# Optimization experiments

Measured on AMD Instinct MI355X. Metric: run time of the kernel, lower is better.

## Reference

```python
import jax, jax.numpy as jnp
import numpy as np

EPS = 1e-12  # matches torch F.normalize default eps

def setup_inputs() -> dict:
    key = jax.random.key(0)
    x = jax.random.normal(key, (8192, 512), dtype=jnp.float32)
    return {"x": x}

def reference(x) -> jnp.ndarray:
    # q = k = v = x, shape [B, C]
    # cosine-similarity scores: L2-normalize rows, then QK^T -> [B, B]
    norm = jnp.maximum(jnp.linalg.norm(x, axis=-1, keepdims=True), EPS)
    xn = x / norm
    attn = xn @ xn.T                      # [B, B] cosine similarities
    attn = jax.nn.softmax(attn, axis=-1)  # row softmax
    out = attn @ x                        # [B, C]
    return out
```

## Files before the change

### kernel.cpp

```cpp
#include <hip/hip_runtime.h>

#define NB 8192
#define ND 512
#define QB 64
#define KB 64
#define NTILES (NB / KB)
#define TILE_BYTES (KB * ND * 2)

typedef unsigned short u16;
typedef unsigned int u32;
typedef __attribute__((ext_vector_type(8))) short bf16x8;
typedef __attribute__((ext_vector_type(4))) float f32x4;

__device__ inline u16 f2bf(float f) {
  u32 u = __float_as_uint(f);
  return (u16)((u + 0x7fffu + ((u >> 16) & 1u)) >> 16);
}

__global__ __launch_bounds__(256) void prep_norms(const float* __restrict__ x,
                                                  float* __restrict__ norms) {
  int row = blockIdx.x * 4 + (threadIdx.x >> 6);
  int lane = threadIdx.x & 63;
  const float4* xr = reinterpret_cast<const float4*>(x + (size_t)row * ND);
  float4 a = xr[lane];
  float4 b = xr[64 + lane];
  float ss = a.x * a.x + a.y * a.y + a.z * a.z + a.w * a.w +
             b.x * b.x + b.y * b.y + b.z * b.z + b.w * b.w;
  ss += __shfl_xor(ss, 1);  ss += __shfl_xor(ss, 2);  ss += __shfl_xor(ss, 4);
  ss += __shfl_xor(ss, 8);  ss += __shfl_xor(ss, 16); ss += __shfl_xor(ss, 32);
  if (lane == 0) norms[row] = 1.0f / fmaxf(sqrtf(ss), 1e-12f);
}

__global__ __launch_bounds__(256) void prep_images(const float* __restrict__ x,
                                                   u16* __restrict__ Kimg,
                                                   u16* __restrict__ Vfrag) {
  __shared__ u16 Lt[KB * ND];
  const int t = blockIdx.x;
  const int tid = threadIdx.x;

  {
    int kv = tid >> 2, d0 = (tid & 3) * 128;
    const float* src = x + (size_t)(t * KB + kv) * ND + d0;
    char* kbase = (char*)Kimg + (size_t)t * TILE_BYTES;
#pragma unroll
    for (int j = 0; j < 16; ++j) {
      float4 f0 = *(const float4*)(src + j * 8);
      float4 f1 = *(const float4*)(src + j * 8 + 4);
      union { u16 u[8]; uint4 v; } pk;
      pk.u[0] = f2bf(f0.x); pk.u[1] = f2bf(f0.y); pk.u[2] = f2bf(f0.z); pk.u[3] = f2bf(f0.w);
      pk.u[4] = f2bf(f1.x); pk.u[5] = f2bf(f1.y); pk.u[6] = f2bf(f1.z); pk.u[7] = f2bf(f1.w);
      int byte = (kv * 1024 + (d0 + j * 8) * 2) ^ ((kv & 7) << 4);
      *(uint4*)(kbase + byte) = pk.v;
      *(uint4*)((char*)Lt + byte) = pk.v;
    }
  }
  __syncthreads();
  {
    char* vbase = (char*)Vfrag + (size_t)t * TILE_BYTES;
#pragma unroll
    for (int i = 0; i < 16; ++i) {
      int gid = tid + 256 * i;
      int d = (gid >> 9) * 64 + (((gid >> 7) & 3) * 16) + (gid & 15);
      int kv0 = ((gid >> 6) & 1) * 32 + ((gid >> 4) & 3) * 8;
      union { u16 u[8]; uint4 v; } o;
#pragma unroll
      for (int k = 0; k < 8; ++k) {
        int sb = ((kv0 + k) * 1024 + d * 2) ^ (((kv0 + k) & 7) << 4);
        o.u[k] = *(const u16*)((const char*)Lt + sb);
      }
      *(uint4*)(vbase + gid * 16) = o.v;
    }
  }
}

template <int NCH>
__global__ __launch_bounds__(512, 2) void attn_kernel(const float* __restrict__ x,
                                                      const u16* __restrict__ Kimg,
                                                      const u16* __restrict__ Vfrag,
                                                      const float* __restrict__ norms,
                                                      float* __restrict__ Opart,
                                                      float* __restrict__ Zpart,
                                                      float* __restrict__ out) {
  __shared__ u16 Kl[2][KB * ND];
  __shared__ u16 Pl[QB * KB];
  __shared__ float Nl[(NCH == 2) ? 4096 : 4];
  __shared__ float Zred[256];
  __shared__ float Zfin[QB];

  const int tid = threadIdx.x;
  const int w = tid >> 6;
  const int l = tid & 63;
  const int bid = blockIdx.x;

  int chunk, qblk;
  if constexpr (NCH == 2) {
    chunk = (bid >> 2) & 1;
    qblk = (bid & 3) * 32 + (bid >> 3);
  } else {
    chunk = 0;
    qblk = (bid & 7) * 16 + (bid >> 3);
  }
  const int CT = NTILES / NCH;
  const int CHUNK = NB / NCH;
  const int tile0 = chunk * CT;

  const int pq = w & 1;
  const int tkv = w >> 1;

  bf16x8 qf[2][16];
#pragma unroll
  for (int a = 0; a < 2; ++a) {
    int qrow = qblk * QB + (pq * 2 + a) * 16 + (l & 15);
    float rnq = norms[qrow];
    const float* xr = x + (size_t)qrow * ND;
#pragma unroll
    for (int ks = 0; ks < 16; ++ks) {
      int d0 = ks * 32 + (l >> 4) * 8;
      float4 f0 = *(const float4*)(xr + d0);
      float4 f1 = *(const float4*)(xr + d0 + 4);
      union { u16 u[8]; bf16x8 v; } pk;
      pk.u[0] = f2bf(f0.x * rnq); pk.u[1] = f2bf(f0.y * rnq);
      pk.u[2] = f2bf(f0.z * rnq); pk.u[3] = f2bf(f0.w * rnq);
      pk.u[4] = f2bf(f1.x * rnq); pk.u[5] = f2bf(f1.y * rnq);
      pk.u[6] = f2bf(f1.z * rnq); pk.u[7] = f2bf(f1.w * rnq);
      qf[a][ks] = pk.v;
    }
  }

  if constexpr (NCH == 2) {
    const float4* ns = (const float4*)(norms + chunk * CHUNK);
    float4 n0 = ns[tid * 2], n1 = ns[tid * 2 + 1];
    *(float4*)&Nl[tid * 8] = n0;
    *(float4*)&Nl[tid * 8 + 4] = n1;
  }

  auto stageK = [&](int tg, int b) {
    size_t toff = (size_t)tg * TILE_BYTES;
#pragma unroll
    for (int j = 0; j < 8; ++j) {
      const char* src = (const char*)Kimg + toff + (w * 8 + j) * 1024 + l * 16;
      char* dst = (char*)&Kl[b][0] + (w * 8 + j) * 1024;
      __builtin_amdgcn_global_load_lds((const void*)src, (void*)dst, 16, 0, 0);
    }
  };

  stageK(tile0, 0);
  asm volatile("s_waitcnt vmcnt(0) lgkmcnt(0)" ::: "memory");
  __builtin_amdgcn_s_barrier();
  __builtin_amdgcn_sched_barrier(0);

  f32x4 oacc[4][4];
#pragma unroll
  for (int a = 0; a < 4; ++a)
#pragma unroll
    for (int b = 0; b < 4; ++b) oacc[a][b] = (f32x4){0.f, 0.f, 0.f, 0.f};
  float za[2] = {0.f, 0.f};

  const int kv = tkv * 16 + (l & 15);
  const int krowbase = kv * 1024;
  const int kswz = (kv & 7) << 4;
  const int hi16 = (l >> 4) * 16;
  const char* vsrc_base = (const char*)Vfrag + (size_t)w * 8192 + (size_t)l * 16;

  for (int t = 0; t < CT; ++t) {
    const int buf = t & 1;

    uint4 vreg[8];
    {
      const char* vs = vsrc_base + (size_t)(tile0 + t) * TILE_BYTES;
#pragma unroll
      for (int j = 0; j < 8; ++j) vreg[j] = *(const uint4*)(vs + j * 1024);
    }
    if (t + 1 < CT) stageK(tile0 + t + 1, buf ^ 1);

    f32x4 acc0 = {0.f, 0.f, 0.f, 0.f}, acc1 = {0.f, 0.f, 0.f, 0.f};
    {
      const char* kb = (const char*)&Kl[buf][0];
#pragma unroll
      for (int ks = 0; ks < 16; ++ks) {
        bf16x8 kf = *(const bf16x8*)(kb + ((krowbase + ks * 64 + hi16) ^ kswz));
        acc0 = __builtin_amdgcn_mfma_f32_16x16x32_bf16(kf, qf[0][ks], acc0, 0, 0, 0);
        acc1 = __builtin_amdgcn_mfma_f32_16x16x32_bf16(kf, qf[1][ks], acc1, 0, 0, 0);
      }
    }
    {
      int kvb = tkv * 16 + (l >> 4) * 4;
      float4 rn4;
      if constexpr (NCH == 2) rn4 = *(const float4*)&Nl[t * KB + kvb];
      else rn4 = *(const float4*)(norms + t * KB + kvb);
#pragma unroll
      for (int a = 0; a < 2; ++a) {
        const f32x4& ac = a ? acc1 : acc0;
        float p0 = __expf(ac[0] * rn4.x);
        float p1 = __expf(ac[1] * rn4.y);
        float p2 = __expf(ac[2] * rn4.z);
        float p3 = __expf(ac[3] * rn4.w);
        za[a] += (p0 + p1) + (p2 + p3);
        u32 w01, w23;
        asm("v_cvt_pk_bf16_f32 %0, %1, %2" : "=v"(w01) : "v"(p0), "v"(p1));
        asm("v_cvt_pk_bf16_f32 %0, %1, %2" : "=v"(w23) : "v"(p2), "v"(p3));
        int q = (pq * 2 + a) * 16 + (l & 15);
        int pbyte = (q * 128 + kvb * 2) ^ ((q & 7) << 4);
        *(uint2*)((char*)Pl + pbyte) = (uint2){w01, w23};
      }
    }
    asm volatile("s_waitcnt lgkmcnt(0)" ::: "memory");
    __builtin_amdgcn_s_barrier();
    __builtin_amdgcn_sched_barrier(0);

    {
      const char* plb = (const char*)Pl;
      bf16x8 pa[4][2];
#pragma unroll
      for (int q2 = 0; q2 < 4; ++q2) {
        int qr = q2 * 16 + (l & 15);
        int qswz = (qr & 7) << 4;
#pragma unroll
        for (int ks = 0; ks < 2; ++ks)
          pa[q2][ks] = *(const bf16x8*)(plb + ((qr * 128 + ks * 64 + hi16) ^ qswz));
      }
#pragma unroll
      for (int dt = 0; dt < 4; ++dt) {
#pragma unroll
        for (int ks = 0; ks < 2; ++ks) {
          union { uint4 q; bf16x8 v; } uu;
          uu.q = vreg[dt * 2 + ks];
#pragma unroll
          for (int q2 = 0; q2 < 4; ++q2)
            oacc[q2][dt] =
                __builtin_amdgcn_mfma_f32_16x16x32_bf16(pa[q2][ks], uu.v, oacc[q2][dt], 0, 0, 0);
        }
      }
    }
    asm volatile("s_waitcnt vmcnt(0) lgkmcnt(0)" ::: "memory");
    __builtin_amdgcn_s_barrier();
    __builtin_amdgcn_sched_barrier(0);
  }

  {
#pragma unroll
    for (int a = 0; a < 2; ++a) {
      float s = za[a];
      s += __shfl_xor(s, 16);
      s += __shfl_xor(s, 32);
      if (l < 16) Zred[w * 32 + a * 16 + l] = s;
    }
  }
  __syncthreads();

  if constexpr (NCH == 2) {
    if (tid < QB) {
      int g = tid >> 4, p_ = g >> 1, a_ = g & 1;
      float s = 0.f;
#pragma unroll
      for (int tk = 0; tk < 4; ++tk) s += Zred[(tk * 2 + p_) * 32 + a_ * 16 + (tid & 15)];
      Zpart[chunk * NB + qblk * QB + tid] = s;
    }
    float* op = Opart + (size_t)chunk * NB * ND;
#pragma unroll
    for (int q2 = 0; q2 < 4; ++q2)
#pragma unroll
      for (int dt = 0; dt < 4; ++dt) {
        int d = w * 64 + dt * 16 + (l & 15);
#pragma unroll
        for (int r = 0; r < 4; ++r) {
          int q = qblk * QB + q2 * 16 + (l >> 4) * 4 + r;
          op[(size_t)q * ND + d] = oacc[q2][dt][r];
        }
      }
  } else {
    if (tid < QB) {
      int g = tid >> 4, p_ = g >> 1, a_ = g & 1;
      float s = 0.f;
#pragma unroll
      for (int tk = 0; tk < 4; ++tk) s += Zred[(tk * 2 + p_) * 32 + a_ * 16 + (tid & 15)];
      Zfin[tid] = s;
    }
    __syncthreads();
#pragma unroll
    for (int q2 = 0; q2 < 4; ++q2) {
      float rz[4];
#pragma unroll
      for (int r = 0; r < 4; ++r) rz[r] = 1.0f / Zfin[q2 * 16 + (l >> 4) * 4 + r];
#pragma unroll
      for (int dt = 0; dt < 4; ++dt) {
        int d = w * 64 + dt * 16 + (l & 15);
#pragma unroll
        for (int r = 0; r < 4; ++r) {
          int q = qblk * QB + q2 * 16 + (l >> 4) * 4 + r;
          out[(size_t)q * ND + d] = oacc[q2][dt][r] * rz[r];
        }
      }
    }
  }
}

__global__ __launch_bounds__(256) void combine_kernel(const float* __restrict__ Opart,
                                                      const float* __restrict__ Zpart,
                                                      float* __restrict__ out) {
  size_t idx = ((size_t)blockIdx.x * 256 + threadIdx.x) * 4;
  int row = (int)(idx >> 9);
  float rz = 1.0f / (Zpart[row] + Zpart[NB + row]);
  float4 a = *(const float4*)(Opart + idx);
  float4 b = *(const float4*)(Opart + (size_t)NB * ND + idx);
  float4 o = {(a.x + b.x) * rz, (a.y + b.y) * rz, (a.z + b.z) * rz, (a.w + b.w) * rz};
  *(float4*)(out + idx) = o;
}

extern "C" void kernel_launch(void* const* d_in, const int* in_sizes, int n_in,
                              void* d_out, int out_size, void* d_ws, size_t ws_size,
                              hipStream_t stream) {
  const float* x = (const float*)d_in[0];
  float* outp = (float*)d_out;

  char* ws = (char*)d_ws;
  const size_t img_bytes = (size_t)NB * ND * 2;
  float* norms = (float*)ws;
  u16* Kimg = (u16*)(ws + 32768);
  u16* Vfrag = (u16*)(ws + 32768 + img_bytes);
  size_t base = 32768 + 2 * img_bytes;
  float* Zpart = (float*)(ws + base);
  float* Opart = (float*)(ws + base + 65536);
  size_t need = base + 65536 + (size_t)2 * NB * ND * 4;

  prep_norms<<<NB / 4, 256, 0, stream>>>(x, norms);
  prep_images<<<NTILES, 256, 0, stream>>>(x, Kimg, Vfrag);
  if (ws_size >= need) {
    attn_kernel<2><<<256, 512, 0, stream>>>(x, Kimg, Vfrag, norms, Opart, Zpart, nullptr);
    combine_kernel<<<(NB * ND) / 1024, 256, 0, stream>>>(Opart, Zpart, outp);
  } else {
    attn_kernel<1><<<128, 512, 0, stream>>>(x, Kimg, Vfrag, norms, nullptr, nullptr, outp);
  }
}
```

Measured before the change: 287.8 us.

## Shrink query block to 32 with 256-thread blocks and single-buffered K tile

Halves the query block to 32 rows and uses 256-thread workgroups, launching twice as many blocks. Each wave now owns 16 KV rows and 128 output columns. K staging drops from double-buffered to single-buffered LDS, with the next-tile prefetch issued after the P barrier. V fragment loads are split into two halves to spread register pressure, and s_setprio is raised around the MFMA loops. The goal is more blocks and lower LDS use for better occupancy, at the cost of half the Q reuse per K/V tile, so K and V are streamed twice as often overall.

```diff
diff --git a/kernel.cpp b/kernel.cpp
--- a/kernel.cpp
+++ b/kernel.cpp
@@ -2,7 +2,7 @@
 
 #define NB 8192
 #define ND 512
-#define QB 64
+#define QB 32
 #define KB 64
 #define NTILES (NB / KB)
 #define TILE_BYTES (KB * ND * 2)
@@ -74,17 +74,16 @@
 }
 
 template <int NCH>
-__global__ __launch_bounds__(512, 2) void attn_kernel(const float* __restrict__ x,
+__global__ __launch_bounds__(256, 2) void attn_kernel(const float* __restrict__ x,
                                                       const u16* __restrict__ Kimg,
                                                       const u16* __restrict__ Vfrag,
                                                       const float* __restrict__ norms,
                                                       float* __restrict__ Opart,
                                                       float* __restrict__ Zpart,
                                                       float* __restrict__ out) {
-  __shared__ u16 Kl[2][KB * ND];
+  __shared__ u16 Kl[KB * ND];
   __shared__ u16 Pl[QB * KB];
-  __shared__ float Nl[(NCH == 2) ? 4096 : 4];
-  __shared__ float Zred[256];
+  __shared__ float Zred[128];
   __shared__ float Zfin[QB];
 
   const int tid = threadIdx.x;
@@ -94,23 +93,20 @@
 
   int chunk, qblk;
   if constexpr (NCH == 2) {
-    chunk = (bid >> 2) & 1;
-    qblk = (bid & 3) * 32 + (bid >> 3);
+    chunk = (bid & 7) >> 2;
+    qblk = (bid >> 3) * 4 + (bid & 3);
   } else {
     chunk = 0;
-    qblk = (bid & 7) * 16 + (bid >> 3);
+    qblk = bid;
   }
   const int CT = NTILES / NCH;
   const int CHUNK = NB / NCH;
   const int tile0 = chunk * CT;
 
-  const int pq = w & 1;
-  const int tkv = w >> 1;
-
   bf16x8 qf[2][16];
 #pragma unroll
   for (int a = 0; a < 2; ++a) {
-    int qrow = qblk * QB + (pq * 2 + a) * 16 + (l & 15);
+    int qrow = qblk * QB + a * 16 + (l & 15);
     float rnq = norms[qrow];
     const float* xr = x + (size_t)qrow * ND;
 #pragma unroll
@@ -127,67 +123,58 @@
     }
   }
 
-  if constexpr (NCH == 2) {
-    const float4* ns = (const float4*)(norms + chunk * CHUNK);
-    float4 n0 = ns[tid * 2], n1 = ns[tid * 2 + 1];
-    *(float4*)&Nl[tid * 8] = n0;
-    *(float4*)&Nl[tid * 8 + 4] = n1;
-  }
-
-  auto stageK = [&](int tg, int b) {
+  auto stageK = [&](int tg) {
     size_t toff = (size_t)tg * TILE_BYTES;
 #pragma unroll
-    for (int j = 0; j < 8; ++j) {
-      const char* src = (const char*)Kimg + toff + (w * 8 + j) * 1024 + l * 16;
-      char* dst = (char*)&Kl[b][0] + (w * 8 + j) * 1024;
+    for (int j = 0; j < 16; ++j) {
+      const char* src = (const char*)Kimg + toff + (tid + 256 * j) * 16;
+      char* dst = (char*)Kl + (tid + 256 * j) * 16;
       __builtin_amdgcn_global_load_lds((const void*)src, (void*)dst, 16, 0, 0);
     }
   };
 
-  stageK(tile0, 0);
+  stageK(tile0);
   asm volatile("s_waitcnt vmcnt(0) lgkmcnt(0)" ::: "memory");
   __builtin_amdgcn_s_barrier();
   __builtin_amdgcn_sched_barrier(0);
 
-  f32x4 oacc[4][4];
-#pragma unroll
-  for (int a = 0; a < 4; ++a)
-#pragma unroll
-    for (int b = 0; b < 4; ++b) oacc[a][b] = (f32x4){0.f, 0.f, 0.f, 0.f};
+  f32x4 oacc[2][8];
+#pragma unroll
+  for (int a = 0; a < 2; ++a)
+#pragma unroll
+    for (int b = 0; b < 8; ++b) oacc[a][b] = (f32x4){0.f, 0.f, 0.f, 0.f};
   float za[2] = {0.f, 0.f};
 
-  const int kv = tkv * 16 + (l & 15);
+  const int kv = w * 16 + (l & 15);
   const int krowbase = kv * 1024;
   const int kswz = (kv & 7) << 4;
   const int hi16 = (l >> 4) * 16;
-  const char* vsrc_base = (const char*)Vfrag + (size_t)w * 8192 + (size_t)l * 16;
+  const char* vsb = (const char*)Vfrag + (size_t)w * 16384 + ((size_t)((l >> 4) * 16 + (l & 15))) * 16;
 
   for (int t = 0; t < CT; ++t) {
-    const int buf = t & 1;
-
-    uint4 vreg[8];
-    {
-      const char* vs = vsrc_base + (size_t)(tile0 + t) * TILE_BYTES;
-#pragma unroll
-      for (int j = 0; j < 8; ++j) vreg[j] = *(const uint4*)(vs + j * 1024);
-    }
-    if (t + 1 < CT) stageK(tile0 + t + 1, buf ^ 1);
+    const char* vs = vsb + (size_t)(tile0 + t) * TILE_BYTES;
+    uint4 vregA[8];
+#pragma unroll
+    for (int dt = 0; dt < 4; ++dt)
+#pragma unroll
+      for (int ks = 0; ks < 2; ++ks)
+        vregA[dt * 2 + ks] = *(const uint4*)(vs + (dt >> 2) * 8192 + (dt & 3) * 2048 + ks * 1024);
 
     f32x4 acc0 = {0.f, 0.f, 0.f, 0.f}, acc1 = {0.f, 0.f, 0.f, 0.f};
     {
-      const char* kb = (const char*)&Kl[buf][0];
+      const char* kb = (const char*)Kl;
+      __builtin_amdgcn_s_setprio(1);
 #pragma unroll
       for (int ks = 0; ks < 16; ++ks) {
         bf16x8 kf = *(const bf16x8*)(kb + ((krowbase + ks * 64 + hi16) ^ kswz));
         acc0 = __builtin_amdgcn_mfma_f32_16x16x32_bf16(kf, qf[0][ks], acc0, 0, 0, 0);
         acc1 = __builtin_amdgcn_mfma_f32_16x16x32_bf16(kf, qf[1][ks], acc1, 0, 0, 0);
       }
+      __builtin_amdgcn_s_setprio(0);
     }
     {
-      int kvb = tkv * 16 + (l >> 4) * 4;
-      float4 rn4;
-      if constexpr (NCH == 2) rn4 = *(const float4*)&Nl[t * KB + kvb];
-      else rn4 = *(const float4*)(norms + t * KB + kvb);
+      int kvb = w * 16 + (l >> 4) * 4;
+      float4 rn4 = *(const float4*)(norms + chunk * CHUNK + t * KB + kvb);
 #pragma unroll
       for (int a = 0; a < 2; ++a) {
         const f32x4& ac = a ? acc1 : acc0;
@@ -199,7 +186,7 @@
         u32 w01, w23;
         asm("v_cvt_pk_bf16_f32 %0, %1, %2" : "=v"(w01) : "v"(p0), "v"(p1));
         asm("v_cvt_pk_bf16_f32 %0, %1, %2" : "=v"(w23) : "v"(p2), "v"(p3));
-        int q = (pq * 2 + a) * 16 + (l & 15);
+        int q = a * 16 + (l & 15);
         int pbyte = (q * 128 + kvb * 2) ^ ((q & 7) << 4);
         *(uint2*)((char*)Pl + pbyte) = (uint2){w01, w23};
       }
@@ -208,29 +195,39 @@
     __builtin_amdgcn_s_barrier();
     __builtin_amdgcn_sched_barrier(0);
 
+    uint4 vregB[8];
+#pragma unroll
+    for (int dt = 4; dt < 8; ++dt)
+#pragma unroll
+      for (int ks = 0; ks < 2; ++ks)
+        vregB[(dt - 4) * 2 + ks] = *(const uint4*)(vs + (dt >> 2) * 8192 + (dt & 3) * 2048 + ks * 1024);
+    if (t + 1 < CT) stageK(tile0 + t + 1);
+
     {
       const char* plb = (const char*)Pl;
-      bf16x8 pa[4][2];
-#pragma unroll
-      for (int q2 = 0; q2 < 4; ++q2) {
-        int qr = q2 * 16 + (l & 15);
+      bf16x8 pa[2][2];
+#pragma unroll
+      for (int a = 0; a < 2; ++a) {
+        int qr = a * 16 + (l & 15);
         int qswz = (qr & 7) << 4;
 #pragma unroll
         for (int ks = 0; ks < 2; ++ks)
-          pa[q2][ks] = *(const bf16x8*)(plb + ((qr * 128 + ks * 64 + hi16) ^ qswz));
-      }
-#pragma unroll
-      for (int dt = 0; dt < 4; ++dt) {
+          pa[a][ks] = *(const bf16x8*)(plb + ((qr * 128 + ks * 64 + hi16) ^ qswz));
+      }
+      __builtin_amdgcn_s_setprio(1);
+#pragma unroll
+      for (int dt = 0; dt < 8; ++dt) {
 #pragma unroll
         for (int ks = 0; ks < 2; ++ks) {
           union { uint4 q; bf16x8 v; } uu;
-          uu.q = vreg[dt * 2 + ks];
-#pragma unroll
-          for (int q2 = 0; q2 < 4; ++q2)
-            oacc[q2][dt] =
-                __builtin_amdgcn_mfma_f32_16x16x32_bf16(pa[q2][ks], uu.v, oacc[q2][dt], 0, 0, 0);
+          uu.q = (dt < 4) ? vregA[dt * 2 + ks] : vregB[(dt - 4) * 2 + ks];
+#pragma unroll
+          for (int a = 0; a < 2; ++a)
+            oacc[a][dt] =
+                __builtin_amdgcn_mfma_f32_16x16x32_bf16(pa[a][ks], uu.v, oacc[a][dt], 0, 0, 0);
         }
       }
+      __builtin_amdgcn_s_setprio(0);
     }
     asm volatile("s_waitcnt vmcnt(0) lgkmcnt(0)" ::: "memory");
     __builtin_amdgcn_s_barrier();
@@ -250,45 +247,43 @@
 
   if constexpr (NCH == 2) {
     if (tid < QB) {
-      int g = tid >> 4, p_ = g >> 1, a_ = g & 1;
       float s = 0.f;
 #pragma unroll
-      for (int tk = 0; tk < 4; ++tk) s += Zred[(tk * 2 + p_) * 32 + a_ * 16 + (tid & 15)];
+      for (int wv = 0; wv < 4; ++wv) s += Zred[wv * 32 + tid];
       Zpart[chunk * NB + qblk * QB + tid] = s;
     }
     float* op = Opart + (size_t)chunk * NB * ND;
 #pragma unroll
-    for (int q2 = 0; q2 < 4; ++q2)
-#pragma unroll
-      for (int dt = 0; dt < 4; ++dt) {
-        int d = w * 64 + dt * 16 + (l & 15);
+    for (int a = 0; a < 2; ++a)
+#pragma unroll
+      for (int dt = 0; dt < 8; ++dt) {
+        int d = w * 128 + dt * 16 + (l & 15);
 #pragma unroll
         for (int r = 0; r < 4; ++r) {
-          int q = qblk * QB + q2 * 16 + (l >> 4) * 4 + r;
-          op[(size_t)q * ND + d] = oacc[q2][dt][r];
+          int q = qblk * QB + a * 16 + (l >> 4) * 4 + r;
+          op[(size_t)q * ND + d] = oacc[a][dt][r];
         }
       }
   } else {
     if (tid < QB) {
-      int g = tid >> 4, p_ = g >> 1, a_ = g & 1;
       float s = 0.f;
 #pragma unroll
-      for (int tk = 0; tk < 4; ++tk) s += Zred[(tk * 2 + p_) * 32 + a_ * 16 + (tid & 15)];
+      for (int wv = 0; wv < 4; ++wv) s += Zred[wv * 32 + tid];
       Zfin[tid] = s;
     }
     __syncthreads();
 #pragma unroll
-    for (int q2 = 0; q2 < 4; ++q2) {
+    for (int a = 0; a < 2; ++a) {
       float rz[4];
 #pragma unroll
-      for (int r = 0; r < 4; ++r) rz[r] = 1.0f / Zfin[q2 * 16 + (l >> 4) * 4 + r];
-#pragma unroll
-      for (int dt = 0; dt < 4; ++dt) {
-        int d = w * 64 + dt * 16 + (l & 15);
+      for (int r = 0; r < 4; ++r) rz[r] = 1.0f / Zfin[a * 16 + (l >> 4) * 4 + r];
+#pragma unroll
+      for (int dt = 0; dt < 8; ++dt) {
+        int d = w * 128 + dt * 16 + (l & 15);
 #pragma unroll
         for (int r = 0; r < 4; ++r) {
-          int q = qblk * QB + q2 * 16 + (l >> 4) * 4 + r;
-          out[(size_t)q * ND + d] = oacc[q2][dt][r] * rz[r];
+          int q = qblk * QB + a * 16 + (l >> 4) * 4 + r;
+          out[(size_t)q * ND + d] = oacc[a][dt][r] * rz[r];
         }
       }
     }
@@ -326,9 +321,9 @@
   prep_norms<<<NB / 4, 256, 0, stream>>>(x, norms);
   prep_images<<<NTILES, 256, 0, stream>>>(x, Kimg, Vfrag);
   if (ws_size >= need) {
-    attn_kernel<2><<<256, 512, 0, stream>>>(x, Kimg, Vfrag, norms, Opart, Zpart, nullptr);
+    attn_kernel<2><<<512, 256, 0, stream>>>(x, Kimg, Vfrag, norms, Opart, Zpart, nullptr);
     combine_kernel<<<(NB * ND) / 1024, 256, 0, stream>>>(Opart, Zpart, outp);
   } else {
-    attn_kernel<1><<<128, 512, 0, stream>>>(x, Kimg, Vfrag, norms, nullptr, nullptr, outp);
-  }
-}
+    attn_kernel<1><<<256, 256, 0, stream>>>(x, Kimg, Vfrag, norms, nullptr, nullptr, outp);
+  }
+}
```

After: 529.7 us. 1.84x slower.

## Split KV into four chunks, single-buffer K in LDS, store bf16 partials

Applied to the files above, without the earlier changes.

Adds a four-way KV split with 512 blocks so more CUs are busy, and stores the partial outputs as bf16 to halve the write and read traffic of the combine step. K staging goes from double-buffered to single-buffered LDS, with the next tile's load issued after the score barrier, which cuts LDS use and may allow more occupancy. The per-chunk norm cache in LDS is dropped, and s_setprio is wrapped around the MFMA loops. The risks are that single buffering exposes K load latency, and that bf16 partial sums lose precision.

```diff
diff --git a/kernel.cpp b/kernel.cpp
--- a/kernel.cpp
+++ b/kernel.cpp
@@ -16,6 +16,7 @@
   u32 u = __float_as_uint(f);
   return (u16)((u + 0x7fffu + ((u >> 16) & 1u)) >> 16);
 }
+__device__ inline float bf2f(u16 u) { return __uint_as_float(((u32)u) << 16); }
 
 __global__ __launch_bounds__(256) void prep_norms(const float* __restrict__ x,
                                                   float* __restrict__ norms) {
@@ -78,12 +79,11 @@
                                                       const u16* __restrict__ Kimg,
                                                       const u16* __restrict__ Vfrag,
                                                       const float* __restrict__ norms,
-                                                      float* __restrict__ Opart,
+                                                      u16* __restrict__ Opart,
                                                       float* __restrict__ Zpart,
                                                       float* __restrict__ out) {
-  __shared__ u16 Kl[2][KB * ND];
+  __shared__ u16 Kl[KB * ND];
   __shared__ u16 Pl[QB * KB];
-  __shared__ float Nl[(NCH == 2) ? 4096 : 4];
   __shared__ float Zred[256];
   __shared__ float Zfin[QB];
 
@@ -93,12 +93,15 @@
   const int bid = blockIdx.x;
 
   int chunk, qblk;
-  if constexpr (NCH == 2) {
-    chunk = (bid >> 2) & 1;
-    qblk = (bid & 3) * 32 + (bid >> 3);
+  if constexpr (NCH == 4) {
+    chunk = (bid & 7) >> 1;
+    qblk = (bid >> 3) * 2 + (bid & 1);
+  } else if constexpr (NCH == 2) {
+    chunk = (bid & 7) >> 2;
+    qblk = (bid >> 3) * 4 + (bid & 3);
   } else {
     chunk = 0;
-    qblk = (bid & 7) * 16 + (bid >> 3);
+    qblk = bid;
   }
   const int CT = NTILES / NCH;
   const int CHUNK = NB / NCH;
@@ -127,24 +130,17 @@
     }
   }
 
-  if constexpr (NCH == 2) {
-    const float4* ns = (const float4*)(norms + chunk * CHUNK);
-    float4 n0 = ns[tid * 2], n1 = ns[tid * 2 + 1];
-    *(float4*)&Nl[tid * 8] = n0;
-    *(float4*)&Nl[tid * 8 + 4] = n1;
-  }
-
-  auto stageK = [&](int tg, int b) {
+  auto stageK = [&](int tg) {
     size_t toff = (size_t)tg * TILE_BYTES;
 #pragma unroll
     for (int j = 0; j < 8; ++j) {
       const char* src = (const char*)Kimg + toff + (w * 8 + j) * 1024 + l * 16;
-      char* dst = (char*)&Kl[b][0] + (w * 8 + j) * 1024;
+      char* dst = (char*)Kl + (w * 8 + j) * 1024;
       __builtin_amdgcn_global_load_lds((const void*)src, (void*)dst, 16, 0, 0);
     }
   };
 
-  stageK(tile0, 0);
+  stageK(tile0);
   asm volatile("s_waitcnt vmcnt(0) lgkmcnt(0)" ::: "memory");
   __builtin_amdgcn_s_barrier();
   __builtin_amdgcn_sched_barrier(0);
@@ -163,31 +159,28 @@
   const char* vsrc_base = (const char*)Vfrag + (size_t)w * 8192 + (size_t)l * 16;
 
   for (int t = 0; t < CT; ++t) {
-    const int buf = t & 1;
-
     uint4 vreg[8];
     {
       const char* vs = vsrc_base + (size_t)(tile0 + t) * TILE_BYTES;
 #pragma unroll
       for (int j = 0; j < 8; ++j) vreg[j] = *(const uint4*)(vs + j * 1024);
     }
-    if (t + 1 < CT) stageK(tile0 + t + 1, buf ^ 1);
 
     f32x4 acc0 = {0.f, 0.f, 0.f, 0.f}, acc1 = {0.f, 0.f, 0.f, 0.f};
     {
-      const char* kb = (const char*)&Kl[buf][0];
+      const char* kb = (const char*)Kl;
+      __builtin_amdgcn_s_setprio(1);
 #pragma unroll
       for (int ks = 0; ks < 16; ++ks) {
         bf16x8 kf = *(const bf16x8*)(kb + ((krowbase + ks * 64 + hi16) ^ kswz));
         acc0 = __builtin_amdgcn_mfma_f32_16x16x32_bf16(kf, qf[0][ks], acc0, 0, 0, 0);
         acc1 = __builtin_amdgcn_mfma_f32_16x16x32_bf16(kf, qf[1][ks], acc1, 0, 0, 0);
       }
+      __builtin_amdgcn_s_setprio(0);
     }
     {
       int kvb = tkv * 16 + (l >> 4) * 4;
-      float4 rn4;
-      if constexpr (NCH == 2) rn4 = *(const float4*)&Nl[t * KB + kvb];
-      else rn4 = *(const float4*)(norms + t * KB + kvb);
+      float4 rn4 = *(const float4*)(norms + chunk * CHUNK + t * KB + kvb);
 #pragma unroll
       for (int a = 0; a < 2; ++a) {
         const f32x4& ac = a ? acc1 : acc0;
@@ -208,6 +201,8 @@
     __builtin_amdgcn_s_barrier();
     __builtin_amdgcn_sched_barrier(0);
 
+    if (t + 1 < CT) stageK(tile0 + t + 1);
+
     {
       const char* plb = (const char*)Pl;
       bf16x8 pa[4][2];
@@ -219,6 +214,7 @@
         for (int ks = 0; ks < 2; ++ks)
           pa[q2][ks] = *(const bf16x8*)(plb + ((qr * 128 + ks * 64 + hi16) ^ qswz));
       }
+      __builtin_amdgcn_s_setprio(1);
 #pragma unroll
       for (int dt = 0; dt < 4; ++dt) {
 #pragma unroll
@@ -231,6 +227,7 @@
                 __builtin_amdgcn_mfma_f32_16x16x32_bf16(pa[q2][ks], uu.v, oacc[q2][dt], 0, 0, 0);
         }
       }
+      __builtin_amdgcn_s_setprio(0);
     }
     asm volatile("s_waitcnt vmcnt(0) lgkmcnt(0)" ::: "memory");
     __builtin_amdgcn_s_barrier();
@@ -248,7 +245,7 @@
   }
   __syncthreads();
 
-  if constexpr (NCH == 2) {
+  if constexpr (NCH > 1) {
     if (tid < QB) {
       int g = tid >> 4, p_ = g >> 1, a_ = g & 1;
       float s = 0.f;
@@ -256,7 +253,7 @@
       for (int tk = 0; tk < 4; ++tk) s += Zred[(tk * 2 + p_) * 32 + a_ * 16 + (tid & 15)];
       Zpart[chunk * NB + qblk * QB + tid] = s;
     }
-    float* op = Opart + (size_t)chunk * NB * ND;
+    u16* op = Opart + (size_t)chunk * NB * ND;
 #pragma unroll
     for (int q2 = 0; q2 < 4; ++q2)
 #pragma unroll
@@ -265,7 +262,7 @@
 #pragma unroll
         for (int r = 0; r < 4; ++r) {
           int q = qblk * QB + q2 * 16 + (l >> 4) * 4 + r;
-          op[(size_t)q * ND + d] = oacc[q2][dt][r];
+          op[(size_t)q * ND + d] = f2bf(oacc[q2][dt][r]);
         }
       }
   } else {
@@ -295,16 +292,24 @@
   }
 }
 
-__global__ __launch_bounds__(256) void combine_kernel(const float* __restrict__ Opart,
+template <int NCH>
+__global__ __launch_bounds__(256) void combine_kernel(const u16* __restrict__ Opart,
                                                       const float* __restrict__ Zpart,
                                                       float* __restrict__ out) {
   size_t idx = ((size_t)blockIdx.x * 256 + threadIdx.x) * 4;
   int row = (int)(idx >> 9);
-  float rz = 1.0f / (Zpart[row] + Zpart[NB + row]);
-  float4 a = *(const float4*)(Opart + idx);
-  float4 b = *(const float4*)(Opart + (size_t)NB * ND + idx);
-  float4 o = {(a.x + b.x) * rz, (a.y + b.y) * rz, (a.z + b.z) * rz, (a.w + b.w) * rz};
-  *(float4*)(out + idx) = o;
+  float z = 0.f;
+#pragma unroll
+  for (int c = 0; c < NCH; ++c) z += Zpart[c * NB + row];
+  float rz = 1.0f / z;
+  float4 o = {0.f, 0.f, 0.f, 0.f};
+#pragma unroll
+  for (int c = 0; c < NCH; ++c) {
+    ushort4 v = *(const ushort4*)(Opart + (size_t)c * NB * ND + idx);
+    o.x += bf2f(v.x); o.y += bf2f(v.y); o.z += bf2f(v.z); o.w += bf2f(v.w);
+  }
+  float4 r = {o.x * rz, o.y * rz, o.z * rz, o.w * rz};
+  *(float4*)(out + idx) = r;
 }
 
 extern "C" void kernel_launch(void* const* d_in, const int* in_sizes, int n_in,
@@ -320,14 +325,18 @@
   u16* Vfrag = (u16*)(ws + 32768 + img_bytes);
   size_t base = 32768 + 2 * img_bytes;
   float* Zpart = (float*)(ws + base);
-  float* Opart = (float*)(ws + base + 65536);
-  size_t need = base + 65536 + (size_t)2 * NB * ND * 4;
+  u16* Opart = (u16*)(ws + base + 131072);
+  size_t need4 = base + 131072 + (size_t)4 * NB * ND * 2;
+  size_t need2 = base + 131072 + (size_t)2 * NB * ND * 2;
 
   prep_norms<<<NB / 4, 256, 0, stream>>>(x, norms);
   prep_images<<<NTILES, 256, 0, stream>>>(x, Kimg, Vfrag);
-  if (ws_size >= need) {
+  if (ws_size >= need4) {
+    attn_kernel<4><<<512, 512, 0, stream>>>(x, Kimg, Vfrag, norms, Opart, Zpart, nullptr);
+    combine_kernel<4><<<(NB * ND) / 1024, 256, 0, stream>>>(Opart, Zpart, outp);
+  } else if (ws_size >= need2) {
     attn_kernel<2><<<256, 512, 0, stream>>>(x, Kimg, Vfrag, norms, Opart, Zpart, nullptr);
-    combine_kernel<<<(NB * ND) / 1024, 256, 0, stream>>>(Opart, Zpart, outp);
+    combine_kernel<2><<<(NB * ND) / 1024, 256, 0, stream>>>(Opart, Zpart, outp);
   } else {
     attn_kernel<1><<<128, 512, 0, stream>>>(x, Kimg, Vfrag, norms, nullptr, nullptr, outp);
   }
```

Measured after the change: 392.3 us. 36.3% more time.
